# Kernel optimization log

Measured on AMD Instinct MI355X. Metric: run time of the kernel, lower is better.

Reference implementation:

```python
import jax, jax.numpy as jnp
import numpy as np

NUM_EXPERTS = 8
TOP_K = 2

def setup_inputs() -> dict:
    key = jax.random.key(0)
    ks = jax.random.split(key, 5)
    B, S, D, E, H = 4, 2048, 1024, NUM_EXPERTS, 4096
    scale = 0.02
    return {
        'x': jax.random.normal(ks[0], (B, S, D), dtype=jnp.float32),
        'router_w': jax.random.normal(ks[1], (D, E), dtype=jnp.float32) * scale,
        'router_b': jnp.zeros((E,), dtype=jnp.float32),
        'w1': jax.random.normal(ks[2], (E, D, H), dtype=jnp.float32) * scale,
        'b1': jnp.zeros((E, H), dtype=jnp.float32),
        'w2': jax.random.normal(ks[3], (E, H, D), dtype=jnp.float32) * scale,
        'b2': jnp.zeros((E, D), dtype=jnp.float32),
    }

def reference(x, router_w, router_b, w1, b1, w2, b2):
    B, S, D = x.shape
    E = router_b.shape[0]
    x_flat = x.reshape(-1, D)                       # [T, D], T = B*S
    logits = x_flat @ router_w + router_b          # [T, E]
    routing_weights = jax.nn.softmax(logits, axis=-1)
    # NOTE: original module computes & renormalizes top-k weights but never
    # applies them — outputs of selected experts are summed UNWEIGHTED.
    top_w, top_idx = jax.lax.top_k(routing_weights, TOP_K)  # [T, k]
    out_flat = jnp.zeros_like(x_flat)
    for e in range(E):  # fixed small expert count; dense compute + mask combine
        mask = jnp.any(top_idx == e, axis=-1)      # [T]
        h = jax.nn.gelu(x_flat @ w1[e] + b1[e], approximate=False)  # [T, H]
        y = h @ w2[e] + b2[e]                      # [T, D]
        out_flat = out_flat + jnp.where(mask[:, None], y, 0.0)
    return out_flat.reshape(B, S, D)
```

## Files before the change

kernel.cpp:

```cpp
#include <hip/hip_runtime.h>

#define T_TOKENS 8192
#define DIM 1024
#define NEXP 8
#define HID 4096
#define ROWS (2 * T_TOKENS)
#define ROWS_PAD (ROWS + 128)

#define META_COUNTS 0
#define META_OFFSET 16
#define META_TOP2   32
#define META_ROWPOS (32 + T_TOKENS)

typedef __attribute__((ext_vector_type(8))) short short8;
typedef __attribute__((ext_vector_type(4))) float f32x4;
typedef __attribute__((ext_vector_type(4))) unsigned short u16x4;

__device__ __forceinline__ unsigned short bf16bits(float f) {
  unsigned u = __builtin_bit_cast(unsigned, f);
  u += 0x7fffu + ((u >> 16) & 1u);
  return (unsigned short)(u >> 16);
}

__device__ __forceinline__ void gl_lds16(const void* g, void* l) {
  __builtin_amdgcn_global_load_lds(
      (const __attribute__((address_space(1))) unsigned int*)g,
      (__attribute__((address_space(3))) unsigned int*)l, 16, 0, 0);
}

__global__ __launch_bounds__(256) void transpose_w_kernel(
    const float* __restrict__ in, unsigned short* __restrict__ out, int R, int C) {
  __shared__ float tile[32][33];
  const int e = blockIdx.z;
  const int r0 = blockIdx.y * 32, c0 = blockIdx.x * 32;
  const float* inp = in + (size_t)e * R * C;
  unsigned short* outp = out + (size_t)e * R * C;
  const int tr = threadIdx.x >> 5, tc = threadIdx.x & 31;
#pragma unroll
  for (int s = 0; s < 32; s += 8)
    tile[tr + s][tc] = inp[(size_t)(r0 + tr + s) * C + (c0 + tc)];
  __syncthreads();
#pragma unroll
  for (int s = 0; s < 32; s += 8)
    outp[(size_t)(c0 + tr + s) * R + (r0 + tc)] = bf16bits(tile[tc][tr + s]);
}

__global__ __launch_bounds__(256) void router_kernel(
    const float* __restrict__ x, const float* __restrict__ rw,
    const float* __restrict__ rb, int* __restrict__ meta) {
  const int w = threadIdx.x >> 6;
  const int l = threadIdx.x & 63;
  const int t = blockIdx.x * 4 + w;
  const float* xr = x + (size_t)t * DIM + l * 16;
  double acc[8];
#pragma unroll
  for (int e = 0; e < 8; ++e) acc[e] = 0.0;
#pragma unroll
  for (int m = 0; m < 16; m += 4) {
    f32x4 xv = *(const f32x4*)(xr + m);
#pragma unroll
    for (int q = 0; q < 4; ++q) {
      double xs = (double)xv[q];
      const float* rwr = rw + (size_t)(l * 16 + m + q) * NEXP;
      f32x4 r0 = *(const f32x4*)rwr;
      f32x4 r1 = *(const f32x4*)(rwr + 4);
      acc[0] += xs * (double)r0[0]; acc[1] += xs * (double)r0[1];
      acc[2] += xs * (double)r0[2]; acc[3] += xs * (double)r0[3];
      acc[4] += xs * (double)r1[0]; acc[5] += xs * (double)r1[1];
      acc[6] += xs * (double)r1[2]; acc[7] += xs * (double)r1[3];
    }
  }
#pragma unroll
  for (int off = 32; off >= 1; off >>= 1) {
#pragma unroll
    for (int e = 0; e < 8; ++e) acc[e] += __shfl_down(acc[e], off);
  }
  if (l == 0) {
    double lg[8];
#pragma unroll
    for (int e = 0; e < 8; ++e) lg[e] = acc[e] + (double)rb[e];
    int e1 = 0; double b1v = lg[0];
#pragma unroll
    for (int e = 1; e < 8; ++e) if (lg[e] > b1v) { b1v = lg[e]; e1 = e; }
    int e2 = -1; double b2v = -1e300;
#pragma unroll
    for (int e = 0; e < 8; ++e) if (e != e1 && lg[e] > b2v) { b2v = lg[e]; e2 = e; }
    meta[META_TOP2 + t] = e1 | (e2 << 4);
  }
}

__global__ __launch_bounds__(1024) void assign_kernel(int* __restrict__ meta) {
  __shared__ int hist[NEXP][1024];
  __shared__ int own[NEXP][1024];
  const int tid = threadIdx.x;
#pragma unroll
  for (int e = 0; e < NEXP; ++e) { hist[e][tid] = 0; own[e][tid] = 0; }
  __syncthreads();
  int top2[8];
#pragma unroll
  for (int q = 0; q < 8; ++q) {
    int t = tid * 8 + q;
    int p = meta[META_TOP2 + t];
    top2[q] = p;
    hist[p & 15][tid] += 1;
    hist[(p >> 4) & 15][tid] += 1;
  }
#pragma unroll
  for (int e = 0; e < NEXP; ++e) own[e][tid] = hist[e][tid];
  __syncthreads();
  for (int off = 1; off < 1024; off <<= 1) {
    int add[NEXP];
#pragma unroll
    for (int e = 0; e < NEXP; ++e) add[e] = (tid >= off) ? hist[e][tid - off] : 0;
    __syncthreads();
#pragma unroll
    for (int e = 0; e < NEXP; ++e) hist[e][tid] += add[e];
    __syncthreads();
  }
  int offp[NEXP];
  {
    int o = 0;
#pragma unroll
    for (int e = 0; e < NEXP; ++e) {
      offp[e] = o;
      o += hist[e][1023];
    }
  }
  if (tid == 0) {
#pragma unroll
    for (int e = 0; e < NEXP; ++e) {
      meta[META_COUNTS + e] = hist[e][1023];
      meta[META_OFFSET + e] = offp[e];
    }
  }
#pragma unroll
  for (int e = 0; e < NEXP; ++e) own[e][tid] = offp[e] + hist[e][tid] - own[e][tid];
#pragma unroll
  for (int q = 0; q < 8; ++q) {
    int t = tid * 8 + q;
    int p = top2[q];
    int e1 = p & 15, e2 = (p >> 4) & 15;
    int r1 = own[e1][tid]; own[e1][tid] = r1 + 1;
    int r2 = own[e2][tid]; own[e2][tid] = r2 + 1;
    meta[META_ROWPOS + 2 * t] = r1;
    meta[META_ROWPOS + 2 * t + 1] = r2;
  }
}

__global__ __launch_bounds__(256) void gather_kernel(
    const float* __restrict__ x, unsigned short* __restrict__ gx,
    const int* __restrict__ meta) {
  const int t = blockIdx.x;
  const int r1 = meta[META_ROWPOS + 2 * t];
  const int r2 = meta[META_ROWPOS + 2 * t + 1];
  const int i = threadIdx.x * 4;
  f32x4 v = *(const f32x4*)(x + (size_t)t * DIM + i);
  u16x4 u;
  u[0] = bf16bits(v[0]); u[1] = bf16bits(v[1]);
  u[2] = bf16bits(v[2]); u[3] = bf16bits(v[3]);
  *(u16x4*)(gx + (size_t)r1 * DIM + i) = u;
  *(u16x4*)(gx + (size_t)r2 * DIM + i) = u;
}

template <int ACT>
__global__ __launch_bounds__(256) void moe_gemm(
    const unsigned short* __restrict__ A, const unsigned short* __restrict__ Bt,
    const float* __restrict__ bias, void* __restrict__ C,
    const int* __restrict__ meta, int K, int N) {
  const int e = blockIdx.z;
  const int n_e = meta[META_COUNTS + e];
  const int mt = blockIdx.y;
  if (mt * 128 >= n_e) return;
  const int n0 = blockIdx.x * 128;
  const int row0 = meta[META_OFFSET + e] + mt * 128;
  const int mrem = n_e - mt * 128;

  __shared__ __align__(16) unsigned short As[128 * 64];
  __shared__ __align__(16) unsigned short Bs[128 * 64];

  const int tid = threadIdx.x;
  const int w = tid >> 6, l = tid & 63;
  const int wr = w >> 1, wc = w & 1;

  f32x4 acc[4][4] = {};

  const unsigned short* Bte = Bt + (size_t)e * N * K;

  for (int kt = 0; kt < K; kt += 64) {
#pragma unroll
    for (int it = 0; it < 4; ++it) {
      int idx = it * 2048 + tid * 8;
      int row = idx >> 6;
      int cp = (idx >> 3) & 7;
      int col = ((cp ^ (row & 7)) << 3);
      gl_lds16(A + (size_t)(row0 + row) * K + kt + col, &As[it * 2048 + w * 512]);
    }
#pragma unroll
    for (int it = 0; it < 4; ++it) {
      int idx = it * 2048 + tid * 8;
      int row = idx >> 6;
      int cp = (idx >> 3) & 7;
      int col = ((cp ^ (row & 7)) << 3);
      gl_lds16(Bte + (size_t)(n0 + row) * K + kt + col, &Bs[it * 2048 + w * 512]);
    }
    __syncthreads();
#pragma unroll
    for (int ks = 0; ks < 2; ++ks) {
      short8 av[4], bv[4];
#pragma unroll
      for (int i = 0; i < 4; ++i) {
        int r = wr * 64 + i * 16 + (l & 15);
        int c = ks * 4 + (l >> 4);
        av[i] = *(const short8*)&As[r * 64 + ((c ^ (r & 7)) << 3)];
      }
#pragma unroll
      for (int j = 0; j < 4; ++j) {
        int r = wc * 64 + j * 16 + (l & 15);
        int c = ks * 4 + (l >> 4);
        bv[j] = *(const short8*)&Bs[r * 64 + ((c ^ (r & 7)) << 3)];
      }
#pragma unroll
      for (int i = 0; i < 4; ++i)
#pragma unroll
        for (int j = 0; j < 4; ++j)
          acc[i][j] = __builtin_amdgcn_mfma_f32_16x16x32_bf16(av[i], bv[j], acc[i][j], 0, 0, 0);
    }
    __syncthreads();
  }

  const int lc = l & 15;
  const int lro = (l >> 4) << 2;
#pragma unroll
  for (int i = 0; i < 4; ++i) {
#pragma unroll
    for (int j = 0; j < 4; ++j) {
      int gn = n0 + wc * 64 + j * 16 + lc;
      float bz = bias[(size_t)e * N + gn];
#pragma unroll
      for (int r = 0; r < 4; ++r) {
        int lr = wr * 64 + i * 16 + lro + r;
        if (lr < mrem) {
          float v = acc[i][j][r] + bz;
          size_t off = (size_t)(row0 + lr) * N + gn;
          if (ACT == 1) {
            v = 0.5f * v * (1.0f + erff(v * 0.70710678118654752f));
            ((unsigned short*)C)[off] = bf16bits(v);
          } else {
            ((float*)C)[off] = v;
          }
        }
      }
    }
  }
}

__global__ __launch_bounds__(256) void combine_kernel(
    const float* __restrict__ y, const int* __restrict__ meta, float* __restrict__ out) {
  const int t = blockIdx.x;
  const int r1 = meta[META_ROWPOS + 2 * t];
  const int r2 = meta[META_ROWPOS + 2 * t + 1];
  const int i = threadIdx.x * 4;
  f32x4 a = *(const f32x4*)(y + (size_t)r1 * DIM + i);
  f32x4 b = *(const f32x4*)(y + (size_t)r2 * DIM + i);
  f32x4 o = a + b;
  *(f32x4*)(out + (size_t)t * DIM + i) = o;
}

extern "C" void kernel_launch(void* const* d_in, const int* in_sizes, int n_in,
                              void* d_out, int out_size, void* d_ws, size_t ws_size,
                              hipStream_t stream) {
  const float* x  = (const float*)d_in[0];
  const float* rw = (const float*)d_in[1];
  const float* rb = (const float*)d_in[2];
  const float* w1 = (const float*)d_in[3];
  const float* b1 = (const float*)d_in[4];
  const float* w2 = (const float*)d_in[5];
  const float* b2 = (const float*)d_in[6];
  float* out = (float*)d_out;

  char* p = (char*)d_ws;
  unsigned short* w1t = (unsigned short*)p; p += (size_t)NEXP * DIM * HID * 2;
  unsigned short* w2t = (unsigned short*)p; p += (size_t)NEXP * DIM * HID * 2;
  unsigned short* gx  = (unsigned short*)p; p += (size_t)ROWS_PAD * DIM * 2;
  unsigned short* h   = (unsigned short*)p; p += (size_t)ROWS_PAD * HID * 2;
  float*          y   = (float*)p;          p += (size_t)ROWS_PAD * DIM * 4;
  int*            meta = (int*)p;
  (void)in_sizes; (void)n_in; (void)out_size; (void)ws_size;

  transpose_w_kernel<<<dim3(HID / 32, DIM / 32, NEXP), 256, 0, stream>>>(w1, w1t, DIM, HID);
  transpose_w_kernel<<<dim3(DIM / 32, HID / 32, NEXP), 256, 0, stream>>>(w2, w2t, HID, DIM);

  router_kernel<<<T_TOKENS / 4, 256, 0, stream>>>(x, rw, rb, meta);
  assign_kernel<<<1, 1024, 0, stream>>>(meta);
  gather_kernel<<<T_TOKENS, 256, 0, stream>>>(x, gx, meta);

  moe_gemm<1><<<dim3(HID / 128, 64, NEXP), 256, 0, stream>>>(gx, w1t, b1, h, meta, DIM, HID);
  moe_gemm<0><<<dim3(DIM / 128, 64, NEXP), 256, 0, stream>>>(h, w2t, b2, y, meta, HID, DIM);

  combine_kernel<<<T_TOKENS, 256, 0, stream>>>(y, meta, out);
}
```

Measured before the change: 610.0 us.

## Use 256x256 double-buffered MoE GEMM tiles with interleaved staging and tanh GELU

Result: slower. 731.9 us (+20.0%).

```diff
diff --git a/kernel.cpp b/kernel.cpp
--- a/kernel.cpp
+++ b/kernel.cpp
@@ -5,7 +5,7 @@
 #define NEXP 8
 #define HID 4096
 #define ROWS (2 * T_TOKENS)
-#define ROWS_PAD (ROWS + 128)
+#define ROWS_PAD (ROWS + 256)
 
 #define META_COUNTS 0
 #define META_OFFSET 16
@@ -26,6 +26,16 @@
   __builtin_amdgcn_global_load_lds(
       (const __attribute__((address_space(1))) unsigned int*)g,
       (__attribute__((address_space(3))) unsigned int*)l, 16, 0, 0);
+}
+
+__device__ __forceinline__ float gelu_tanh(float x) {
+  float x3 = x * x * x;
+  float z = 0.7978845608028654f * x + 0.035677408136300125f * x3;
+  float az = fabsf(z);
+  float e = exp2f(az * 2.885390081777927f);
+  float t = 1.0f - 2.0f / (1.0f + e);
+  t = copysignf(t, z);
+  return 0.5f * x * (1.0f + t);
 }
 
 __global__ __launch_bounds__(256) void transpose_w_kernel(
@@ -121,10 +131,7 @@
   {
     int o = 0;
 #pragma unroll
-    for (int e = 0; e < NEXP; ++e) {
-      offp[e] = o;
-      o += hist[e][1023];
-    }
+    for (int e = 0; e < NEXP; ++e) { offp[e] = o; o += hist[e][1023]; }
   }
   if (tid == 0) {
 #pragma unroll
@@ -163,88 +170,148 @@
 }
 
 template <int ACT>
-__global__ __launch_bounds__(256) void moe_gemm(
+__global__ __launch_bounds__(512) void moe_gemm256(
     const unsigned short* __restrict__ A, const unsigned short* __restrict__ Bt,
     const float* __restrict__ bias, void* __restrict__ C,
     const int* __restrict__ meta, int K, int N) {
   const int e = blockIdx.z;
   const int n_e = meta[META_COUNTS + e];
   const int mt = blockIdx.y;
-  if (mt * 128 >= n_e) return;
-  const int n0 = blockIdx.x * 128;
-  const int row0 = meta[META_OFFSET + e] + mt * 128;
-  const int mrem = n_e - mt * 128;
-
-  __shared__ __align__(16) unsigned short As[128 * 64];
-  __shared__ __align__(16) unsigned short Bs[128 * 64];
+  if (mt * 256 >= n_e) return;
+  const int n0 = blockIdx.x * 256;
+  const int row0 = meta[META_OFFSET + e] + mt * 256;
+  const int mrem = n_e - mt * 256;
+  const int NT = K >> 6;
+
+  __shared__ __align__(16) unsigned short As[2][256 * 64];
+  __shared__ __align__(16) unsigned short Bs[2][256 * 64];
 
   const int tid = threadIdx.x;
-  const int w = tid >> 6, l = tid & 63;
-  const int wr = w >> 1, wc = w & 1;
-
-  f32x4 acc[4][4] = {};
-
-  const unsigned short* Bte = Bt + (size_t)e * N * K;
-
-  for (int kt = 0; kt < K; kt += 64) {
-#pragma unroll
-    for (int it = 0; it < 4; ++it) {
-      int idx = it * 2048 + tid * 8;
-      int row = idx >> 6;
-      int cp = (idx >> 3) & 7;
-      int col = ((cp ^ (row & 7)) << 3);
-      gl_lds16(A + (size_t)(row0 + row) * K + kt + col, &As[it * 2048 + w * 512]);
-    }
-#pragma unroll
-    for (int it = 0; it < 4; ++it) {
-      int idx = it * 2048 + tid * 8;
-      int row = idx >> 6;
-      int cp = (idx >> 3) & 7;
-      int col = ((cp ^ (row & 7)) << 3);
-      gl_lds16(Bte + (size_t)(n0 + row) * K + kt + col, &Bs[it * 2048 + w * 512]);
-    }
-    __syncthreads();
-#pragma unroll
-    for (int ks = 0; ks < 2; ++ks) {
-      short8 av[4], bv[4];
-#pragma unroll
-      for (int i = 0; i < 4; ++i) {
-        int r = wr * 64 + i * 16 + (l & 15);
-        int c = ks * 4 + (l >> 4);
-        av[i] = *(const short8*)&As[r * 64 + ((c ^ (r & 7)) << 3)];
-      }
-#pragma unroll
-      for (int j = 0; j < 4; ++j) {
-        int r = wc * 64 + j * 16 + (l & 15);
-        int c = ks * 4 + (l >> 4);
-        bv[j] = *(const short8*)&Bs[r * 64 + ((c ^ (r & 7)) << 3)];
-      }
-#pragma unroll
-      for (int i = 0; i < 4; ++i)
-#pragma unroll
-        for (int j = 0; j < 4; ++j)
-          acc[i][j] = __builtin_amdgcn_mfma_f32_16x16x32_bf16(av[i], bv[j], acc[i][j], 0, 0, 0);
-    }
-    __syncthreads();
+  const int wid = tid >> 6, l = tid & 63;
+  const int wm = wid >> 2, wn = wid & 3;
+  const int rA = l & 15;
+  const int cq = l >> 4;
+
+  const unsigned short* Ag = A + (size_t)row0 * K;
+  const unsigned short* Bg = Bt + (size_t)e * N * K + (size_t)n0 * K;
+
+  size_t aoff[2]; int ldsoff[2];
+#pragma unroll
+  for (int s = 0; s < 2; ++s) {
+    int idx = s * 4096 + tid * 8;
+    int r = idx >> 6;
+    int cp = (idx >> 3) & 7;
+    int col = ((cp ^ (r & 7)) << 3);
+    aoff[s] = (size_t)r * K + col;
+    ldsoff[s] = s * 4096 + (wid << 9);
+  }
+  auto stage_half = [&](const unsigned short* g, unsigned short* lb, int half, int kt) {
+#pragma unroll
+    for (int s = 0; s < 2; ++s)
+      gl_lds16(g + (size_t)half * 128 * K + kt + aoff[s], lb + half * 8192 + ldsoff[s]);
+  };
+  auto stage_hh = [&](int tile, int hh) {
+    if (tile >= NT) return;
+    int kt = tile << 6;
+    if (hh < 2) stage_half(Bg, Bs[tile & 1], hh, kt);
+    else        stage_half(Ag, As[tile & 1], hh - 2, kt);
+  };
+  auto lds_frag = [&](const unsigned short* buf, int r, int chunk) -> short8 {
+    return *(const short8*)&buf[r * 64 + ((chunk ^ (r & 7)) << 3)];
+  };
+
+  stage_hh(0, 0); stage_hh(0, 1); stage_hh(0, 2); stage_hh(0, 3);
+  stage_hh(1, 0); stage_hh(1, 1); stage_hh(1, 2);
+  asm volatile("s_waitcnt vmcnt(6)" ::: "memory");
+  __builtin_amdgcn_s_barrier();
+
+  f32x4 acc[8][4] = {};
+
+  for (int t = 0; t < NT; ++t) {
+    const unsigned short* Ac = As[t & 1];
+    const unsigned short* Bc = Bs[t & 1];
+    short8 b0[4], b1[4], a0lo[4], a0hi[4], a1lo[4], a1hi[4];
+#pragma unroll
+    for (int j = 0; j < 4; ++j) {
+      int r = wn * 64 + j * 16 + rA;
+      b0[j] = lds_frag(Bc, r, cq);
+      b1[j] = lds_frag(Bc, r, 4 + cq);
+    }
+#pragma unroll
+    for (int m = 0; m < 4; ++m)
+      a0lo[m] = lds_frag(Ac, wm * 128 + m * 16 + rA, cq);
+    stage_hh(t + 1, 3);
+    __builtin_amdgcn_s_barrier();
+    asm volatile("s_waitcnt lgkmcnt(0)" ::: "memory");
+    __builtin_amdgcn_s_setprio(1);
+#pragma unroll
+    for (int m = 0; m < 4; ++m)
+#pragma unroll
+      for (int j = 0; j < 4; ++j)
+        acc[m][j] = __builtin_amdgcn_mfma_f32_16x16x32_bf16(a0lo[m], b0[j], acc[m][j], 0, 0, 0);
+    __builtin_amdgcn_s_setprio(0);
+    __builtin_amdgcn_s_barrier();
+#pragma unroll
+    for (int m = 0; m < 4; ++m) {
+      a0hi[m] = lds_frag(Ac, wm * 128 + (m + 4) * 16 + rA, cq);
+      a1lo[m] = lds_frag(Ac, wm * 128 + m * 16 + rA, 4 + cq);
+    }
+    stage_hh(t + 2, 0);
+    __builtin_amdgcn_s_barrier();
+    asm volatile("s_waitcnt lgkmcnt(0)" ::: "memory");
+    __builtin_amdgcn_s_setprio(1);
+#pragma unroll
+    for (int m = 0; m < 4; ++m)
+#pragma unroll
+      for (int j = 0; j < 4; ++j)
+        acc[m + 4][j] = __builtin_amdgcn_mfma_f32_16x16x32_bf16(a0hi[m], b0[j], acc[m + 4][j], 0, 0, 0);
+    __builtin_amdgcn_s_setprio(0);
+    __builtin_amdgcn_s_barrier();
+#pragma unroll
+    for (int m = 0; m < 4; ++m)
+      a1hi[m] = lds_frag(Ac, wm * 128 + (m + 4) * 16 + rA, 4 + cq);
+    stage_hh(t + 2, 1);
+    __builtin_amdgcn_s_barrier();
+    asm volatile("s_waitcnt lgkmcnt(0)" ::: "memory");
+    __builtin_amdgcn_s_setprio(1);
+#pragma unroll
+    for (int m = 0; m < 4; ++m)
+#pragma unroll
+      for (int j = 0; j < 4; ++j)
+        acc[m][j] = __builtin_amdgcn_mfma_f32_16x16x32_bf16(a1lo[m], b1[j], acc[m][j], 0, 0, 0);
+    __builtin_amdgcn_s_setprio(0);
+    __builtin_amdgcn_s_barrier();
+    stage_hh(t + 2, 2);
+    __builtin_amdgcn_s_barrier();
+    asm volatile("s_waitcnt lgkmcnt(0)" ::: "memory");
+    __builtin_amdgcn_s_setprio(1);
+#pragma unroll
+    for (int m = 0; m < 4; ++m)
+#pragma unroll
+      for (int j = 0; j < 4; ++j)
+        acc[m + 4][j] = __builtin_amdgcn_mfma_f32_16x16x32_bf16(a1hi[m], b1[j], acc[m + 4][j], 0, 0, 0);
+    __builtin_amdgcn_s_setprio(0);
+    if (t < NT - 2) { asm volatile("s_waitcnt vmcnt(6)" ::: "memory"); }
+    else            { asm volatile("s_waitcnt vmcnt(0)" ::: "memory"); }
+    __builtin_amdgcn_s_barrier();
   }
 
   const int lc = l & 15;
   const int lro = (l >> 4) << 2;
 #pragma unroll
-  for (int i = 0; i < 4; ++i) {
+  for (int m = 0; m < 8; ++m) {
 #pragma unroll
     for (int j = 0; j < 4; ++j) {
-      int gn = n0 + wc * 64 + j * 16 + lc;
+      int gn = n0 + wn * 64 + j * 16 + lc;
       float bz = bias[(size_t)e * N + gn];
 #pragma unroll
       for (int r = 0; r < 4; ++r) {
-        int lr = wr * 64 + i * 16 + lro + r;
+        int lr = wm * 128 + m * 16 + lro + r;
         if (lr < mrem) {
-          float v = acc[i][j][r] + bz;
+          float v = acc[m][j][r] + bz;
           size_t off = (size_t)(row0 + lr) * N + gn;
           if (ACT == 1) {
-            v = 0.5f * v * (1.0f + erff(v * 0.70710678118654752f));
-            ((unsigned short*)C)[off] = bf16bits(v);
+            ((unsigned short*)C)[off] = bf16bits(gelu_tanh(v));
           } else {
             ((float*)C)[off] = v;
           }
@@ -294,8 +361,8 @@
   assign_kernel<<<1, 1024, 0, stream>>>(meta);
   gather_kernel<<<T_TOKENS, 256, 0, stream>>>(x, gx, meta);
 
-  moe_gemm<1><<<dim3(HID / 128, 64, NEXP), 256, 0, stream>>>(gx, w1t, b1, h, meta, DIM, HID);
-  moe_gemm<0><<<dim3(DIM / 128, 64, NEXP), 256, 0, stream>>>(h, w2t, b2, y, meta, HID, DIM);
+  moe_gemm256<1><<<dim3(HID / 256, 32, NEXP), 512, 0, stream>>>(gx, w1t, b1, h, meta, DIM, HID);
+  moe_gemm256<0><<<dim3(DIM / 256, 32, NEXP), 512, 0, stream>>>(h, w2t, b2, y, meta, HID, DIM);
 
   combine_kernel<<<T_TOKENS, 256, 0, stream>>>(y, meta, out);
 }
```
